# Kernel optimization log

Measured on AMD Instinct MI355X. Metric: run time of the kernel, lower is better.

## Reference

```python
import jax, jax.numpy as jnp
import numpy as np

DIM = 64
NB = 32
LEFT, RIGHT = -1.0, 1.0
EPS_BIN = 0.01
EPS_SLOPE = 0.01


def setup_inputs() -> dict:
    key = jax.random.key(0)
    ks = jax.random.split(key, 10)
    m, cdim, hid = 16384, 64, 100
    x = jax.random.uniform(ks[0], (m, DIM), minval=LEFT + 1e-3, maxval=RIGHT - 1e-3)
    cond = jax.random.normal(ks[1], (m, cdim))
    def dense(k, i, o, scale=1.0):
        return (jax.random.normal(k, (i, o)) * (scale / np.sqrt(i))).astype(jnp.float32)
    inp = dict(
        x=x, cond=cond,
        periodic_mask=jnp.ones((1, DIM), dtype=jnp.int32),
        w_W1=dense(ks[2], cdim, hid), w_b1=jnp.zeros((hid,), jnp.float32),
        w_W2=dense(ks[3], hid, DIM * NB, 0.1), w_b2=jnp.zeros((DIM * NB,), jnp.float32),
        h_W1=dense(ks[4], cdim, hid), h_b1=jnp.zeros((hid,), jnp.float32),
        h_W2=dense(ks[5], hid, DIM * NB, 0.1), h_b2=jnp.zeros((DIM * NB,), jnp.float32),
        s_W1=dense(ks[6], cdim, hid), s_b1=jnp.zeros((hid,), jnp.float32),
        s_W2=dense(ks[7], hid, DIM * (NB + 1), 0.1), s_b2=jnp.zeros((DIM * (NB + 1),), jnp.float32),
    )
    return inp


def _mlp(c, W1, b1, W2, b2):
    return jax.nn.silu(c @ W1 + b1) @ W2 + b2


def _rq_spline(x, w_logit, h_logit, d_raw, periodic_mask):
    # x: [m, dim]; w/h: [m, dim, NB]; d: [m, dim, NB+1]
    widths = EPS_BIN + (1.0 - EPS_BIN * NB) * jax.nn.softmax(w_logit, axis=-1)
    heights = EPS_BIN + (1.0 - EPS_BIN * NB) * jax.nn.softmax(h_logit, axis=-1)
    derivs = EPS_SLOPE + jax.nn.softplus(d_raw)  # [m, dim, NB+1]
    # periodic dims: tie boundary slopes (last == first)
    pm = periodic_mask.astype(bool)  # [1, dim]
    derivs = derivs.at[..., -1].set(jnp.where(pm, derivs[..., 0], derivs[..., -1]))

    span = RIGHT - LEFT
    cw = LEFT + span * jnp.concatenate(
        [jnp.zeros_like(widths[..., :1]), jnp.cumsum(widths, axis=-1)], axis=-1)
    ch = LEFT + span * jnp.concatenate(
        [jnp.zeros_like(heights[..., :1]), jnp.cumsum(heights, axis=-1)], axis=-1)
    cw = cw.at[..., 0].set(LEFT).at[..., -1].set(RIGHT)
    ch = ch.at[..., 0].set(LEFT).at[..., -1].set(RIGHT)
    wk_all = cw[..., 1:] - cw[..., :-1]   # actual bin widths
    hk_all = ch[..., 1:] - ch[..., :-1]   # actual bin heights

    # bin search: number of interior knots <= x
    idx = jnp.sum((x[..., None] >= cw[..., 1:-1]).astype(jnp.int32), axis=-1)
    idx = jnp.clip(idx, 0, NB - 1)[..., None]  # [m, dim, 1]

    gather = lambda a: jnp.take_along_axis(a, idx, axis=-1)[..., 0]
    cwk = gather(cw[..., :-1])
    chk = gather(ch[..., :-1])
    wk = gather(wk_all)
    hk = gather(hk_all)
    dk = gather(derivs[..., :-1])
    dk1 = gather(derivs[..., 1:])

    delta = hk / wk
    theta = (x - cwk) / wk
    t1m = theta * (1.0 - theta)
    denom = delta + (dk1 + dk - 2.0 * delta) * t1m
    y = chk + hk * (delta * theta * theta + dk * t1m) / denom
    deriv = (delta * delta) * (dk1 * theta * theta + 2.0 * delta * t1m
                               + dk * (1.0 - theta) * (1.0 - theta)) / (denom * denom)
    ladJ = jnp.sum(jnp.log(deriv), axis=-1, keepdims=True)  # [m, 1]
    return y, ladJ


def reference(x, cond, periodic_mask, w_W1, w_b1, w_W2, w_b2,
              h_W1, h_b1, h_W2, h_b2, s_W1, s_b1, s_W2, s_b2):
    m = x.shape[0]
    w = _mlp(cond, w_W1, w_b1, w_W2, w_b2).reshape(m, DIM, NB)
    h = _mlp(cond, h_W1, h_b1, h_W2, h_b2).reshape(m, DIM, NB)
    s = _mlp(cond, s_W1, s_b1, s_W2, s_b2).reshape(m, DIM, NB + 1)
    return _rq_spline(x, w, h, s, periodic_mask)
```

## Files before the change

### kernel.cpp

```cpp
#include <hip/hip_runtime.h>
#include <hip/hip_fp16.h>
#include <stdint.h>

#define M_TOTAL 16384
#define DIMS    64
#define CDIM    64
#define HID     100
#define ROWS    32
#define LOG2E   1.4426950408889634f
#define LN2     0.6931471805599453f

typedef __bf16 bf16x8 __attribute__((ext_vector_type(8)));
typedef float  f32x4  __attribute__((ext_vector_type(4)));

#define BKG        14
#define CN_STRIDE  (BKG*16*8)
#define DIM_STRIDE (7*CN_STRIDE)
#define W2M_ELEMS  (DIMS*DIM_STRIDE)
#define B2ALL_ELEMS (DIMS*128)
#define W1M_ELEMS  (3*7*8*16*8)
#define B1_ELEMS   (3*112)
#define W2M_OFF   0
#define B2ALL_OFF (W2M_ELEMS*2)
#define W1M_OFF   (B2ALL_OFF + B2ALL_ELEMS*4)
#define B1_OFF    (W1M_OFF + W1M_ELEMS*2)
#define PART_OFF  1682944

__device__ __forceinline__ uint16_t f2bf(float f) {
  uint32_t u = __float_as_uint(f);
  return (uint16_t)((u + 0x8000u) >> 16);
}

__global__ void repack_kernel(
    const float* __restrict__ wW2, const float* __restrict__ wb2,
    const float* __restrict__ hW2, const float* __restrict__ hb2,
    const float* __restrict__ sW2, const float* __restrict__ sb2,
    const float* __restrict__ wW1, const float* __restrict__ hW1,
    const float* __restrict__ sW1,
    const float* __restrict__ wb1, const float* __restrict__ hb1,
    const float* __restrict__ sb1,
    uint16_t* __restrict__ W2m, float* __restrict__ b2all,
    uint16_t* __restrict__ W1m, float* __restrict__ b1all)
{
  int i = blockIdx.x * 256 + threadIdx.x;
  if (i < W2M_ELEMS) {
    int j  = i & 7;
    int c  = (i >> 3) & 15;
    int t  = i >> 7;
    int kg = t % BKG;
    int t2 = t / BKG;
    int cn = t2 % 7;
    int d  = t2 / 7;
    int k   = kg*8 + j;
    int col = cn*16 + c;
    float v = 0.f;
    if (k < HID) {
      if (col < 32)      v = wW2[k*2048 + d*32 + col] * LOG2E;
      else if (col < 64) v = hW2[k*2048 + d*32 + (col-32)] * LOG2E;
      else if (col < 97) v = sW2[k*2112 + d*33 + (col-64)];
    }
    W2m[i] = f2bf(v);
    return;
  }
  i -= W2M_ELEMS;
  if (i < B2ALL_ELEMS) {
    int c = i & 127;
    int d = i >> 7;
    float v = 0.f;
    if (c < 32)      v = wb2[d*32 + c] * LOG2E;
    else if (c < 64) v = hb2[d*32 + (c-32)] * LOG2E;
    else if (c < 97) v = sb2[d*33 + (c-64)];
    b2all[i] = v;
    return;
  }
  i -= B2ALL_ELEMS;
  if (i < W1M_ELEMS) {
    int jj = i & 7;
    int c  = (i >> 3) & 15;
    int kg = (i >> 7) & 7;
    int t  = i >> 10;
    int cn = t % 7;
    int mat = t / 7;
    int j = cn*16 + c;
    int k = kg*8 + jj;
    const float* W1 = (mat == 0) ? wW1 : (mat == 1) ? hW1 : sW1;
    W1m[i] = f2bf((j < HID) ? W1[k*HID + j] : 0.f);
    return;
  }
  i -= W1M_ELEMS;
  if (i < B1_ELEMS) {
    int mat = i / 112, col = i % 112;
    const float* b1 = (mat == 0) ? wb1 : (mat == 1) ? hb1 : sb1;
    b1all[i] = (col < HID) ? b1[col] : 0.f;
  }
}

__global__ void ladj_reduce(const float* __restrict__ part, float* __restrict__ LADJ) {
  int i = blockIdx.x * 256 + threadIdx.x;
  if (i < M_TOTAL) LADJ[i] = LN2 * (part[i] + part[M_TOTAL + i]);
}

__global__ __launch_bounds__(256, 3)
void spline_main(
    const float* __restrict__ X, const float* __restrict__ C,
    const int* __restrict__ pmask,
    const uint16_t* __restrict__ W2m, const float* __restrict__ b2all,
    const uint16_t* __restrict__ W1m, const float* __restrict__ b1all,
    float* __restrict__ Y, float* __restrict__ part)
{
  __shared__ union {
    float cond_s[ROWS*68];
    __half Ls[4][ROWS*100];
  } U;
  __shared__ uint16_t At[3*13*ROWS*8];
  __shared__ float LjLds[4][ROWS];

  const int tid = threadIdx.x;
  const int rg = blockIdx.x >> 1;
  const int dhalf = blockIdx.x & 1;
  const int r0 = rg * ROWS;
  const int lane = tid & 63, wv = tid >> 6;
  const int l15 = lane & 15, lkg = lane >> 4;
  const int hb = lane >> 5;
  const int srow = lane & 31;

  for (int i = tid; i < ROWS*CDIM; i += 256) {
    int r = i >> 6, c = i & 63;
    U.cond_s[r*68 + c] = C[(size_t)(r0 + r)*CDIM + c];
  }
  __syncthreads();

  {
    bf16x8 cf[2][2];
#pragma unroll
    for (int m = 0; m < 2; ++m)
#pragma unroll
      for (int ks = 0; ks < 2; ++ks) {
        const float* cp = &U.cond_s[(m*16 + l15)*68 + ks*32 + lkg*8];
        float4 c0 = *(const float4*)cp;
        float4 c1 = *(const float4*)(cp + 4);
        union { uint16_t u[8]; bf16x8 v; } tmp;
        tmp.u[0]=f2bf(c0.x); tmp.u[1]=f2bf(c0.y); tmp.u[2]=f2bf(c0.z); tmp.u[3]=f2bf(c0.w);
        tmp.u[4]=f2bf(c1.x); tmp.u[5]=f2bf(c1.y); tmp.u[6]=f2bf(c1.z); tmp.u[7]=f2bf(c1.w);
        cf[m][ks] = tmp.v;
      }
    for (int t = wv; t < 21; t += 4) {
      int mat = t / 7, cn = t % 7;
      const uint16_t* Wb = W1m + (size_t)(mat*7 + cn)*1024;
      bf16x8 wf[2];
#pragma unroll
      for (int ks = 0; ks < 2; ++ks)
        wf[ks] = *(const bf16x8*)&Wb[(ks*4 + lkg)*128 + l15*8];
      f32x4 h0 = {0.f,0.f,0.f,0.f}, h1 = {0.f,0.f,0.f,0.f};
#pragma unroll
      for (int ks = 0; ks < 2; ++ks) {
        h0 = __builtin_amdgcn_mfma_f32_16x16x32_bf16(cf[0][ks], wf[ks], h0, 0, 0, 0);
        h1 = __builtin_amdgcn_mfma_f32_16x16x32_bf16(cf[1][ks], wf[ks], h1, 0, 0, 0);
      }
      float bb = b1all[mat*112 + cn*16 + l15];
      int j = cn*16 + l15;
      if ((j >> 3) <= 12) {
        int base = mat*3328 + (j >> 3)*256 + (j & 7);
#pragma unroll
        for (int r = 0; r < 4; ++r) {
          float a0 = h0[r] + bb;
          float v0 = a0 * __builtin_amdgcn_rcpf(1.f + __builtin_amdgcn_exp2f(-LOG2E*a0));
          At[base + (lkg*4 + r)*8] = f2bf(v0);
          float a1 = h1[r] + bb;
          float v1 = a1 * __builtin_amdgcn_rcpf(1.f + __builtin_amdgcn_exp2f(-LOG2E*a1));
          At[base + (16 + lkg*4 + r)*8] = f2bf(v1);
        }
      }
    }
  }
  __syncthreads();

  __half* LsW = &U.Ls[wv][0];
  const int dbase = dhalf*32 + wv*8;
  float ladj2 = 0.f;
  float xq = 0.f; int pq = 0;

  auto SPLINE = [&](int d, float xv, int pm) {
    const __half* Lr = LsW + srow*100 + hb*32;
    float e[32];
#pragma unroll
    for (int q = 0; q < 16; ++q) {
      __half2 hp = *(const __half2*)(Lr + 2*q);
      float2 f2 = __half22float2(hp);
      e[2*q] = f2.x; e[2*q+1] = f2.y;
    }
    float t2[16], t4[8], t8[4], t16[2];
#pragma unroll
    for (int k = 0; k < 16; ++k) t2[k] = e[2*k] + e[2*k+1];
#pragma unroll
    for (int k = 0; k < 8; ++k)  t4[k] = t2[2*k] + t2[2*k+1];
#pragma unroll
    for (int k = 0; k < 4; ++k)  t8[k] = t4[2*k] + t4[2*k+1];
    t16[0] = t8[0] + t8[1]; t16[1] = t8[2] + t8[3];
    float S = t16[0] + t16[1];
    float rs = __builtin_amdgcn_rcpf(S);
    float Aa = (xv + 1.f) * 0.7352941176470588f * S;
    float Uq = 0.014705882352941176f * S;

    float T = Aa, p = 0.f, fidx;
    {
      float A = fmaf(-16.f, Uq, T);
      bool c4 = t16[0] <= A;
      p = c4 ? t16[0] : p;  T = c4 ? A : T;

      float n8 = c4 ? t8[2] : t8[0];
      A = fmaf(-8.f, Uq, T);
      float tt = p + n8;
      bool c3 = tt <= A;
      p = c3 ? tt : p;  T = c3 ? A : T;

      float n4 = c4 ? (c3 ? t4[6] : t4[4]) : (c3 ? t4[2] : t4[0]);
      A = fmaf(-4.f, Uq, T);
      tt = p + n4;
      bool c2 = tt <= A;
      p = c2 ? tt : p;  T = c2 ? A : T;

      float n2 = c4 ? (c3 ? (c2 ? t2[14] : t2[12]) : (c2 ? t2[10] : t2[8]))
                    : (c3 ? (c2 ? t2[6]  : t2[4])  : (c2 ? t2[2]  : t2[0]));
      A = fmaf(-2.f, Uq, T);
      tt = p + n2;
      bool c1 = tt <= A;
      p = c1 ? tt : p;  T = c1 ? A : T;

      float n1 = c4 ? (c3 ? (c2 ? (c1 ? e[30] : e[28]) : (c1 ? e[26] : e[24]))
                          : (c2 ? (c1 ? e[22] : e[20]) : (c1 ? e[18] : e[16])))
                    : (c3 ? (c2 ? (c1 ? e[14] : e[12]) : (c1 ? e[10] : e[8]))
                          : (c2 ? (c1 ? e[6]  : e[4])  : (c1 ? e[2]  : e[0])));
      A = fmaf(-1.f, Uq, T);
      bool c0 = (p + n1) <= A;
      fidx = (c4 ? 16.f : 0.f) + (c3 ? 8.f : 0.f) + (c2 ? 4.f : 0.f)
           + (c1 ? 2.f : 0.f) + (c0 ? 1.f : 0.f);
    }
    float idxu = __shfl(fidx, srow);
    bool B4 = idxu >= 15.5f; float u = B4 ? idxu - 16.f : idxu;
    bool B3 = u >= 7.5f;  u = B3 ? u - 8.f : u;
    bool B2 = u >= 3.5f;  u = B2 ? u - 4.f : u;
    bool B1 = u >= 1.5f;  u = B1 ? u - 2.f : u;
    bool B0 = u >= 0.5f;
    float Psel = B4 ? t16[0] : 0.f;
    float q8 = B4 ? t8[2] : t8[0];
    Psel = B3 ? Psel + q8 : Psel;
    float q4 = B4 ? (B3 ? t4[6] : t4[4]) : (B3 ? t4[2] : t4[0]);
    Psel = B2 ? Psel + q4 : Psel;
    float q2 = B4 ? (B3 ? (B2 ? t2[14] : t2[12]) : (B2 ? t2[10] : t2[8]))
                  : (B3 ? (B2 ? t2[6]  : t2[4])  : (B2 ? t2[2]  : t2[0]));
    Psel = B1 ? Psel + q2 : Psel;
    float q1e, q1o;
    {
      float a0_ = B1 ? e[2]  : e[0];
      float a1_ = B1 ? e[6]  : e[4];
      float a2_ = B1 ? e[10] : e[8];
      float a3_ = B1 ? e[14] : e[12];
      float a4_ = B1 ? e[18] : e[16];
      float a5_ = B1 ? e[22] : e[20];
      float a6_ = B1 ? e[26] : e[24];
      float a7_ = B1 ? e[30] : e[28];
      float b0_ = B2 ? a1_ : a0_;
      float b1_ = B2 ? a3_ : a2_;
      float b2_ = B2 ? a5_ : a4_;
      float b3_ = B2 ? a7_ : a6_;
      float c0_ = B3 ? b1_ : b0_;
      float c1_ = B3 ? b3_ : b2_;
      q1e = B4 ? c1_ : c0_;
    }
    {
      float a0_ = B1 ? e[3]  : e[1];
      float a1_ = B1 ? e[7]  : e[5];
      float a2_ = B1 ? e[11] : e[9];
      float a3_ = B1 ? e[15] : e[13];
      float a4_ = B1 ? e[19] : e[17];
      float a5_ = B1 ? e[23] : e[21];
      float a6_ = B1 ? e[27] : e[25];
      float a7_ = B1 ? e[31] : e[29];
      float b0_ = B2 ? a1_ : a0_;
      float b1_ = B2 ? a3_ : a2_;
      float b2_ = B2 ? a5_ : a4_;
      float b3_ = B2 ? a7_ : a6_;
      float c0_ = B3 ? b1_ : b0_;
      float c1_ = B3 ? b3_ : b2_;
      q1o = B4 ? c1_ : c0_;
    }
    Psel = B0 ? Psel + q1e : Psel;
    float esel = B0 ? q1o : q1e;

    float cK = fmaf(0.02f, idxu, -1.f) + 1.36f*rs*Psel;
    float wK = (idxu > 30.5f) ? (1.f - cK) : fmaf(1.36f*rs, esel, 0.02f);
    int idxi = (int)idxu;
    int off = 64 + idxi + hb;
    if (hb && idxi == 31) off = pm ? 64 : 96;
    float sl = __half2float(LsW[srow*100 + off]);
    float dkv = fmaf(LN2, __builtin_amdgcn_logf(1.f + __builtin_amdgcn_exp2f(LOG2E*sl)), 0.01f);
    float cO = __shfl_xor(cK, 32);
    float wO = __shfl_xor(wK, 32);
    float dO = __shfl_xor(dkv, 32);
    float cwk = cK, wk = wK, dk = dkv, chk = cO, hk = wO, dk1 = dO;
    float rw = __builtin_amdgcn_rcpf(wk);
    float th = (xv - cwk)*rw;
    float delta = hk*rw;
    float omt = 1.f - th, t1m = th*omt, th2 = th*th;
    float denom = fmaf(dk1 + dk - 2.f*delta, t1m, delta);
    float rden = __builtin_amdgcn_rcpf(denom);
    float yv = fmaf(hk*fmaf(delta, th2, dk*t1m), rden, chk);
    float dn2 = fmaf(dk1, th2, fmaf(2.f*delta, t1m, dk*omt*omt));
    ladj2 += 2.f*(__builtin_amdgcn_logf(delta) - __builtin_amdgcn_logf(denom))
           + __builtin_amdgcn_logf(dn2);
    if (!hb) Y[(size_t)(r0 + srow)*DIMS + d] = yv;
  };

  auto LOADA = [&](bf16x8 (&a2)[2][4], int mat) {
    const uint16_t* base = &At[mat*3328];
#pragma unroll
    for (int m = 0; m < 2; ++m) {
#pragma unroll
      for (int ks = 0; ks < 3; ++ks)
        a2[m][ks] = *(const bf16x8*)&base[(ks*4 + lkg)*256 + (m*16 + l15)*8];
      a2[m][3] = *(const bf16x8*)&base[12*256 + (m*16 + l15)*8];
    }
  };

  auto DO = [&](const bf16x8 (&afm)[2][4], const bf16x8 (&B)[4],
                float bb, int col, bool doexp) {
    f32x4 a0 = {bb,bb,bb,bb}, a1 = {bb,bb,bb,bb};
#pragma unroll
    for (int ks = 0; ks < 4; ++ks)
      a0 = __builtin_amdgcn_mfma_f32_16x16x32_bf16(afm[0][ks], B[ks], a0, 0, 0, 0);
#pragma unroll
    for (int ks = 0; ks < 4; ++ks)
      a1 = __builtin_amdgcn_mfma_f32_16x16x32_bf16(afm[1][ks], B[ks], a1, 0, 0, 0);
    if (doexp) {
#pragma unroll
      for (int r = 0; r < 4; ++r) {
        a0[r] = __builtin_amdgcn_exp2f(a0[r]);
        a1[r] = __builtin_amdgcn_exp2f(a1[r]);
      }
    }
    if (col < 97) {
#pragma unroll
      for (int r = 0; r < 4; ++r) {
        LsW[(lkg*4 + r)*100 + col]      = __float2half(a0[r]);
        LsW[(16 + lkg*4 + r)*100 + col] = __float2half(a1[r]);
      }
    }
  };

#pragma unroll 1
  for (int dd = 0; dd < 8; ++dd) {
    const int d = dbase + dd;
    const uint16_t* Bd = W2m + (size_t)d*DIM_STRIDE;
    auto LOADB = [&](bf16x8 (&dst)[4], int cn) {
#pragma unroll
      for (int ks = 0; ks < 4; ++ks) {
        int kgb = ks*4 + lkg; kgb = (kgb > 13) ? 13 : kgb;
        dst[ks] = *(const bf16x8*)&Bd[cn*CN_STRIDE + kgb*128 + l15*8];
      }
    };
    bf16x8 bA[4], bB[4], bC[4];
    LOADB(bA, 0); LOADB(bB, 1); LOADB(bC, 2);
    float bbv[7];
#pragma unroll
    for (int cn = 0; cn < 7; ++cn) bbv[cn] = b2all[d*128 + cn*16 + l15];
    float xn = X[(size_t)(r0 + srow)*DIMS + d];
    int pn = pmask[d];

    if (dd > 0) SPLINE(d - 1, xq, pq);
    xq = xn; pq = pn;

    bf16x8 afc[2][4];
    LOADA(afc, 0);
    DO(afc, bA, bbv[0], 0*16 + l15, true);  LOADB(bA, 3);
    DO(afc, bB, bbv[1], 1*16 + l15, true);  LOADB(bB, 4);
    LOADA(afc, 1);
    DO(afc, bC, bbv[2], 2*16 + l15, true);  LOADB(bC, 5);
    DO(afc, bA, bbv[3], 3*16 + l15, true);  LOADB(bA, 6);
    LOADA(afc, 2);
    DO(afc, bB, bbv[4], 4*16 + l15, false);
    DO(afc, bC, bbv[5], 5*16 + l15, false);
    DO(afc, bA, bbv[6], 6*16 + l15, false);
  }
  SPLINE(dbase + 7, xq, pq);

  if (!hb) LjLds[wv][srow] = ladj2;
  __syncthreads();
  if (tid < ROWS)
    part[dhalf*M_TOTAL + r0 + tid] =
      (LjLds[0][tid] + LjLds[1][tid]) + (LjLds[2][tid] + LjLds[3][tid]);
}

extern "C" void kernel_launch(void* const* d_in, const int* in_sizes, int n_in,
                              void* d_out, int out_size, void* d_ws, size_t ws_size,
                              hipStream_t stream) {
  const float* x     = (const float*)d_in[0];
  const float* cond  = (const float*)d_in[1];
  const int*   pmask = (const int*)d_in[2];
  const float* wW1 = (const float*)d_in[3];
  const float* wb1 = (const float*)d_in[4];
  const float* wW2 = (const float*)d_in[5];
  const float* wb2 = (const float*)d_in[6];
  const float* hW1 = (const float*)d_in[7];
  const float* hb1 = (const float*)d_in[8];
  const float* hW2 = (const float*)d_in[9];
  const float* hb2 = (const float*)d_in[10];
  const float* sW1 = (const float*)d_in[11];
  const float* sb1 = (const float*)d_in[12];
  const float* sW2 = (const float*)d_in[13];
  const float* sb2 = (const float*)d_in[14];

  uint16_t* W2m   = (uint16_t*)((char*)d_ws + W2M_OFF);
  float*    b2all = (float*)((char*)d_ws + B2ALL_OFF);
  uint16_t* W1m   = (uint16_t*)((char*)d_ws + W1M_OFF);
  float*    b1all = (float*)((char*)d_ws + B1_OFF);
  float*    partp = (float*)((char*)d_ws + PART_OFF);

  const int total = W2M_ELEMS + B2ALL_ELEMS + W1M_ELEMS + B1_ELEMS;
  repack_kernel<<<(total + 255)/256, 256, 0, stream>>>(
      wW2, wb2, hW2, hb2, sW2, sb2, wW1, hW1, sW1, wb1, hb1, sb1,
      W2m, b2all, W1m, b1all);

  float* Y = (float*)d_out;
  float* LADJ = Y + (size_t)M_TOTAL*DIMS;
  spline_main<<<(M_TOTAL/ROWS)*2, 256, 0, stream>>>(
      x, cond, pmask, W2m, b2all, W1m, b1all, Y, partp);
  ladj_reduce<<<(M_TOTAL + 255)/256, 256, 0, stream>>>(partp, LADJ);
}
```

Baseline: 68.78 us.

## Keep third hidden-activation fragment in registers and simplify spline selection and log

The third matrix's SiLU activations are staged through scratch space unioned with the cond buffer, then loaded once into registers (af2), so they are no longer reloaded from LDS on every dimension iteration. The At layout is padded to 16 k-groups, with the padding zeroed explicitly, which removes the special-case indexing. The 32-way select tree for the bin's width entry becomes one indexed half2 LDS load, and three logs collapse into one log of a combined product. This trades more registers, and possible occupancy loss, for fewer LDS reads and ALU ops; the single log could lose some precision.

```diff
diff --git a/kernel.cpp b/kernel.cpp
--- a/kernel.cpp
+++ b/kernel.cpp
@@ -109,10 +109,10 @@
     float* __restrict__ Y, float* __restrict__ part)
 {
   __shared__ union {
-    float cond_s[ROWS*68];
+    struct { float cond_s[ROWS*68]; uint16_t m2scr[16*ROWS*8]; } p;
     __half Ls[4][ROWS*100];
   } U;
-  __shared__ uint16_t At[3*13*ROWS*8];
+  __shared__ uint16_t At[2*16*ROWS*8];
   __shared__ float LjLds[4][ROWS];
 
   const int tid = threadIdx.x;
@@ -126,7 +126,7 @@
 
   for (int i = tid; i < ROWS*CDIM; i += 256) {
     int r = i >> 6, c = i & 63;
-    U.cond_s[r*68 + c] = C[(size_t)(r0 + r)*CDIM + c];
+    U.p.cond_s[r*68 + c] = C[(size_t)(r0 + r)*CDIM + c];
   }
   __syncthreads();
 
@@ -136,7 +136,7 @@
     for (int m = 0; m < 2; ++m)
 #pragma unroll
       for (int ks = 0; ks < 2; ++ks) {
-        const float* cp = &U.cond_s[(m*16 + l15)*68 + ks*32 + lkg*8];
+        const float* cp = &U.p.cond_s[(m*16 + l15)*68 + ks*32 + lkg*8];
         float4 c0 = *(const float4*)cp;
         float4 c1 = *(const float4*)(cp + 4);
         union { uint16_t u[8]; bf16x8 v; } tmp;
@@ -159,20 +159,33 @@
       }
       float bb = b1all[mat*112 + cn*16 + l15];
       int j = cn*16 + l15;
-      if ((j >> 3) <= 12) {
-        int base = mat*3328 + (j >> 3)*256 + (j & 7);
-#pragma unroll
-        for (int r = 0; r < 4; ++r) {
-          float a0 = h0[r] + bb;
-          float v0 = a0 * __builtin_amdgcn_rcpf(1.f + __builtin_amdgcn_exp2f(-LOG2E*a0));
-          At[base + (lkg*4 + r)*8] = f2bf(v0);
-          float a1 = h1[r] + bb;
-          float v1 = a1 * __builtin_amdgcn_rcpf(1.f + __builtin_amdgcn_exp2f(-LOG2E*a1));
-          At[base + (16 + lkg*4 + r)*8] = f2bf(v1);
-        }
-      }
-    }
-  }
+      uint16_t* dst = (mat < 2) ? &At[mat*4096 + (j >> 3)*256 + (j & 7)]
+                                : &U.p.m2scr[(j >> 3)*256 + (j & 7)];
+#pragma unroll
+      for (int r = 0; r < 4; ++r) {
+        float a0 = h0[r] + bb;
+        float v0 = a0 * __builtin_amdgcn_rcpf(1.f + __builtin_amdgcn_exp2f(-LOG2E*a0));
+        dst[(lkg*4 + r)*8] = f2bf(v0);
+        float a1 = h1[r] + bb;
+        float v1 = a1 * __builtin_amdgcn_rcpf(1.f + __builtin_amdgcn_exp2f(-LOG2E*a1));
+        dst[(16 + lkg*4 + r)*8] = f2bf(v1);
+      }
+    }
+    for (int i2 = tid; i2 < 768; i2 += 256) {
+      int reg = i2 >> 8, q = i2 & 255;
+      uint32_t* z = (reg < 2) ? (uint32_t*)&At[reg*4096 + 14*256]
+                              : (uint32_t*)&U.p.m2scr[14*256];
+      z[q] = 0u;
+    }
+  }
+  __syncthreads();
+
+  bf16x8 af2[2][4];
+#pragma unroll
+  for (int m = 0; m < 2; ++m)
+#pragma unroll
+    for (int ks = 0; ks < 4; ++ks)
+      af2[m][ks] = *(const bf16x8*)&U.p.m2scr[(ks*4 + lkg)*256 + (m*16 + l15)*8];
   __syncthreads();
 
   __half* LsW = &U.Ls[wv][0];
@@ -237,6 +250,7 @@
            + (c1 ? 2.f : 0.f) + (c0 ? 1.f : 0.f);
     }
     float idxu = __shfl(fidx, srow);
+    int idxi = (int)idxu;
     bool B4 = idxu >= 15.5f; float u = B4 ? idxu - 16.f : idxu;
     bool B3 = u >= 7.5f;  u = B3 ? u - 8.f : u;
     bool B2 = u >= 3.5f;  u = B2 ? u - 4.f : u;
@@ -250,47 +264,13 @@
     float q2 = B4 ? (B3 ? (B2 ? t2[14] : t2[12]) : (B2 ? t2[10] : t2[8]))
                   : (B3 ? (B2 ? t2[6]  : t2[4])  : (B2 ? t2[2]  : t2[0]));
     Psel = B1 ? Psel + q2 : Psel;
-    float q1e, q1o;
-    {
-      float a0_ = B1 ? e[2]  : e[0];
-      float a1_ = B1 ? e[6]  : e[4];
-      float a2_ = B1 ? e[10] : e[8];
-      float a3_ = B1 ? e[14] : e[12];
-      float a4_ = B1 ? e[18] : e[16];
-      float a5_ = B1 ? e[22] : e[20];
-      float a6_ = B1 ? e[26] : e[24];
-      float a7_ = B1 ? e[30] : e[28];
-      float b0_ = B2 ? a1_ : a0_;
-      float b1_ = B2 ? a3_ : a2_;
-      float b2_ = B2 ? a5_ : a4_;
-      float b3_ = B2 ? a7_ : a6_;
-      float c0_ = B3 ? b1_ : b0_;
-      float c1_ = B3 ? b3_ : b2_;
-      q1e = B4 ? c1_ : c0_;
-    }
-    {
-      float a0_ = B1 ? e[3]  : e[1];
-      float a1_ = B1 ? e[7]  : e[5];
-      float a2_ = B1 ? e[11] : e[9];
-      float a3_ = B1 ? e[15] : e[13];
-      float a4_ = B1 ? e[19] : e[17];
-      float a5_ = B1 ? e[23] : e[21];
-      float a6_ = B1 ? e[27] : e[25];
-      float a7_ = B1 ? e[31] : e[29];
-      float b0_ = B2 ? a1_ : a0_;
-      float b1_ = B2 ? a3_ : a2_;
-      float b2_ = B2 ? a5_ : a4_;
-      float b3_ = B2 ? a7_ : a6_;
-      float c0_ = B3 ? b1_ : b0_;
-      float c1_ = B3 ? b3_ : b2_;
-      q1o = B4 ? c1_ : c0_;
-    }
+    float2 ep = __half22float2(*(const __half2*)(Lr + (idxi & ~1)));
+    float q1e = ep.x, q1o = ep.y;
     Psel = B0 ? Psel + q1e : Psel;
     float esel = B0 ? q1o : q1e;
 
     float cK = fmaf(0.02f, idxu, -1.f) + 1.36f*rs*Psel;
     float wK = (idxu > 30.5f) ? (1.f - cK) : fmaf(1.36f*rs, esel, 0.02f);
-    int idxi = (int)idxu;
     int off = 64 + idxi + hb;
     if (hb && idxi == 31) off = pm ? 64 : 96;
     float sl = __half2float(LsW[srow*100 + off]);
@@ -307,20 +287,17 @@
     float rden = __builtin_amdgcn_rcpf(denom);
     float yv = fmaf(hk*fmaf(delta, th2, dk*t1m), rden, chk);
     float dn2 = fmaf(dk1, th2, fmaf(2.f*delta, t1m, dk*omt*omt));
-    ladj2 += 2.f*(__builtin_amdgcn_logf(delta) - __builtin_amdgcn_logf(denom))
-           + __builtin_amdgcn_logf(dn2);
+    float tq = delta * rden;
+    ladj2 += __builtin_amdgcn_logf(tq*tq*dn2);
     if (!hb) Y[(size_t)(r0 + srow)*DIMS + d] = yv;
   };
 
   auto LOADA = [&](bf16x8 (&a2)[2][4], int mat) {
-    const uint16_t* base = &At[mat*3328];
-#pragma unroll
-    for (int m = 0; m < 2; ++m) {
-#pragma unroll
-      for (int ks = 0; ks < 3; ++ks)
-        a2[m][ks] = *(const bf16x8*)&base[(ks*4 + lkg)*256 + (m*16 + l15)*8];
-      a2[m][3] = *(const bf16x8*)&base[12*256 + (m*16 + l15)*8];
-    }
+#pragma unroll
+    for (int m = 0; m < 2; ++m)
+#pragma unroll
+      for (int ks = 0; ks < 4; ++ks)
+        a2[m][ks] = *(const bf16x8*)&At[mat*4096 + (ks*4 + lkg)*256 + (m*16 + l15)*8];
   };
 
   auto DO = [&](const bf16x8 (&afm)[2][4], const bf16x8 (&B)[4],
@@ -377,10 +354,9 @@
     LOADA(afc, 1);
     DO(afc, bC, bbv[2], 2*16 + l15, true);  LOADB(bC, 5);
     DO(afc, bA, bbv[3], 3*16 + l15, true);  LOADB(bA, 6);
-    LOADA(afc, 2);
-    DO(afc, bB, bbv[4], 4*16 + l15, false);
-    DO(afc, bC, bbv[5], 5*16 + l15, false);
-    DO(afc, bA, bbv[6], 6*16 + l15, false);
+    DO(af2, bB, bbv[4], 4*16 + l15, false);
+    DO(af2, bC, bbv[5], 5*16 + l15, false);
+    DO(af2, bA, bbv[6], 6*16 + l15, false);
   }
   SPLINE(dbase + 7, xq, pq);
 
```

After: 123.5 us. 79.6% more time.
